# Optimization experiments

Hardware: AMD Instinct MI355X
Metric: run time of the kernel (lower is better)

## Reference

```python
import jax, jax.numpy as jnp
import numpy as np

TAU = 2.0   # membrane time constant
V_TH = 0.5  # firing threshold

@jax.custom_vjp
def spike_fn(v):
    return jnp.where(v > 0, 1.0, 0.0)

def _spike_fwd(v):
    return spike_fn(v), v

def _spike_bwd(v, g):
    # atan surrogate gradient (alpha=2): d s / d v = 1 / (1 + (pi*v)^2)
    sg = 1.0 / (1.0 + (jnp.pi * v) ** 2)
    return (g * sg,)

spike_fn.defvjp(_spike_fwd, _spike_bwd)


def setup_inputs() -> dict:
    key = jax.random.key(0)
    # [batch, neurons, time] -- time on axis 2, matching moveaxis(x, 2, 0)
    x = jax.random.normal(key, (32, 16384, 100), dtype=jnp.float32)
    return {"x": x}


def reference(x):
    x_seq = jnp.moveaxis(x, 2, 0)  # [T, B, N]
    decay = 1.0 - 1.0 / TAU

    def scan_fn(v, x_t):
        v = v * decay + x_t            # leaky integrate
        s = spike_fn(v - V_TH)         # fire
        v = v - s * V_TH               # soft reset
        return v, s

    v_init = jnp.zeros_like(x_seq[0])
    _, spikes = jax.lax.scan(scan_fn, v_init, x_seq)
    return jnp.moveaxis(spikes, 0, 2)  # [B, N, T]
```

## Files before the change

### kernel.cpp

```cpp
#include <hip/hip_runtime.h>


#define T_STEPS 100
#define T_VEC   25
#define ROWS    64
#define CA      12
#define CB      13
#define LSTRIDE 13
#define DECAY   0.5f
#define VTH     0.5f

typedef float vfloat4 __attribute__((ext_vector_type(4)));

__global__ __launch_bounds__(64, 3) void lif_kernel(const float* __restrict__ x,
                                                    float* __restrict__ out,
                                                    int n_rows) {
    __shared__ vfloat4 tile[ROWS * LSTRIDE];
    __shared__ unsigned int bits[ROWS * 4];

    const int lane = threadIdx.x;
    const int row0 = blockIdx.x * ROWS;
    const int gf0 = row0 * T_VEC;
    const int total_f4 = n_rows * T_VEC;

    const vfloat4* __restrict__ xb = reinterpret_cast<const vfloat4*>(x);
    const vfloat4 vzero = {0.0f, 0.0f, 0.0f, 0.0f};

    {
        vfloat4 st[CA];
        #pragma unroll
        for (int k = 0; k < CA; ++k) {
            int f = k * 64 + lane;
            int r = f / CA, c = f % CA;
            int g = gf0 + r * T_VEC + c;
            st[k] = (g < total_f4) ? xb[g] : vzero;
        }
        #pragma unroll
        for (int k = 0; k < CA; ++k) {
            int f = k * 64 + lane;
            int r = f / CA, c = f % CA;
            tile[r * LSTRIDE + c] = st[k];
        }
    }
    __syncthreads();

    vfloat4 sb[CB];
    #pragma unroll
    for (int k = 0; k < CB; ++k) {
        int f = k * 64 + lane;
        int r = f / CB, c = f % CB;
        int g = gf0 + r * T_VEC + CA + c;
        sb[k] = (g < total_f4) ? xb[g] : vzero;
    }
    __builtin_amdgcn_sched_barrier(0);

    unsigned int pk0 = 0, pk1 = 0, pk2 = 0, pk3 = 0;
    float v = 0.0f;
    #pragma unroll
    for (int c = 0; c < CA; ++c) {
        vfloat4 xs = tile[lane * LSTRIDE + c];
        #pragma unroll
        for (int k = 0; k < 4; ++k) {
            v = v * DECAY + xs[k];
            bool s = (v - VTH > 0.0f);
            v -= s ? VTH : 0.0f;
            unsigned int bit = s ? 1u : 0u;
            const int b = c * 4 + k;
            if (b < 32) pk0 |= bit << b;
            else        pk1 |= bit << (b - 32);
        }
    }
    __syncthreads();

    #pragma unroll
    for (int k = 0; k < CB; ++k) {
        int f = k * 64 + lane;
        int r = f / CB, c = f % CB;
        tile[r * LSTRIDE + c] = sb[k];
    }
    __syncthreads();

    #pragma unroll
    for (int c = 0; c < CB; ++c) {
        vfloat4 xs = tile[lane * LSTRIDE + c];
        #pragma unroll
        for (int k = 0; k < 4; ++k) {
            v = v * DECAY + xs[k];
            bool s = (v - VTH > 0.0f);
            v -= s ? VTH : 0.0f;
            unsigned int bit = s ? 1u : 0u;
            const int b = 48 + c * 4 + k;
            if (b < 64)      pk1 |= bit << (b - 32);
            else if (b < 96) pk2 |= bit << (b - 64);
            else             pk3 |= bit << (b - 96);
        }
    }

    {
        uint4 w; w.x = pk0; w.y = pk1; w.z = pk2; w.w = pk3;
        reinterpret_cast<uint4*>(bits)[lane] = w;
    }
    __syncthreads();

    vfloat4* __restrict__ ob = reinterpret_cast<vfloat4*>(out);
    #pragma unroll
    for (int i = 0; i < T_VEC; ++i) {
        int f = i * 64 + lane;
        int g = gf0 + f;
        if (g < total_f4) {
            int r  = f / T_VEC;
            int c4 = f % T_VEC;
            unsigned int word = bits[r * 4 + (c4 >> 3)];
            int shift = (c4 & 7) * 4;
            unsigned int nib = (word >> shift) & 0xFu;
            vfloat4 s;
            s.x = (nib & 1u) ? 1.0f : 0.0f;
            s.y = (nib & 2u) ? 1.0f : 0.0f;
            s.z = (nib & 4u) ? 1.0f : 0.0f;
            s.w = (nib & 8u) ? 1.0f : 0.0f;
            ob[g] = s;
        }
    }
}

extern "C" void kernel_launch(void* const* d_in, const int* in_sizes, int n_in,
                              void* d_out, int out_size, void* d_ws, size_t ws_size,
                              hipStream_t stream) {
    const float* x = (const float*)d_in[0];
    float* out = (float*)d_out;

    int n_rows = in_sizes[0] / T_STEPS;
    int grid = (n_rows + ROWS - 1) / ROWS;

    lif_kernel<<<grid, ROWS, 0, stream>>>(x, out, n_rows);
}
```

Baseline: 91.28 us.

## Split LIF into bit-packing walk kernel and separate spike expansion kernel

Splits the single fused kernel into two. The first runs the recurrence and writes packed spike bits per row to the workspace. The second, launched with 256-thread blocks, expands those bits into float output with grid-strided coalesced stores. The aim is to separate the latency-bound serial scan from the bandwidth-bound output write, so each can use its own launch shape. The cost is an extra launch and a round trip through the workspace; the fused path is kept as a fallback when the workspace is too small.

```diff
diff --git a/kernel.cpp b/kernel.cpp
--- a/kernel.cpp
+++ b/kernel.cpp
@@ -12,6 +12,117 @@
 
 typedef float vfloat4 __attribute__((ext_vector_type(4)));
 
+__global__ __launch_bounds__(64, 3) void lif_walk(const float* __restrict__ x,
+                                                  uint4* __restrict__ bitsg,
+                                                  int n_rows) {
+    __shared__ vfloat4 tile[ROWS * LSTRIDE];
+
+    const int lane = threadIdx.x;
+    const int row0 = blockIdx.x * ROWS;
+    const int gf0 = row0 * T_VEC;
+    const int total_f4 = n_rows * T_VEC;
+
+    const vfloat4* __restrict__ xb = reinterpret_cast<const vfloat4*>(x);
+    const vfloat4 vzero = {0.0f, 0.0f, 0.0f, 0.0f};
+
+    {
+        vfloat4 st[CA];
+        #pragma unroll
+        for (int k = 0; k < CA; ++k) {
+            int f = k * 64 + lane;
+            int r = f / CA, c = f % CA;
+            int g = gf0 + r * T_VEC + c;
+            st[k] = (g < total_f4) ? xb[g] : vzero;
+        }
+        #pragma unroll
+        for (int k = 0; k < CA; ++k) {
+            int f = k * 64 + lane;
+            int r = f / CA, c = f % CA;
+            tile[r * LSTRIDE + c] = st[k];
+        }
+    }
+    __syncthreads();
+
+    vfloat4 sb[CB];
+    #pragma unroll
+    for (int k = 0; k < CB; ++k) {
+        int f = k * 64 + lane;
+        int r = f / CB, c = f % CB;
+        int g = gf0 + r * T_VEC + CA + c;
+        sb[k] = (g < total_f4) ? xb[g] : vzero;
+    }
+    __builtin_amdgcn_sched_barrier(0);
+
+    unsigned int pk0 = 0, pk1 = 0, pk2 = 0, pk3 = 0;
+    float v = 0.0f;
+    #pragma unroll
+    for (int c = 0; c < CA; ++c) {
+        vfloat4 xs = tile[lane * LSTRIDE + c];
+        #pragma unroll
+        for (int k = 0; k < 4; ++k) {
+            v = v * DECAY + xs[k];
+            bool s = (v - VTH > 0.0f);
+            v -= s ? VTH : 0.0f;
+            unsigned int bit = s ? 1u : 0u;
+            const int b = c * 4 + k;
+            if (b < 32) pk0 |= bit << b;
+            else        pk1 |= bit << (b - 32);
+        }
+    }
+    __syncthreads();
+
+    #pragma unroll
+    for (int k = 0; k < CB; ++k) {
+        int f = k * 64 + lane;
+        int r = f / CB, c = f % CB;
+        tile[r * LSTRIDE + c] = sb[k];
+    }
+    __syncthreads();
+
+    #pragma unroll
+    for (int c = 0; c < CB; ++c) {
+        vfloat4 xs = tile[lane * LSTRIDE + c];
+        #pragma unroll
+        for (int k = 0; k < 4; ++k) {
+            v = v * DECAY + xs[k];
+            bool s = (v - VTH > 0.0f);
+            v -= s ? VTH : 0.0f;
+            unsigned int bit = s ? 1u : 0u;
+            const int b = 48 + c * 4 + k;
+            if (b < 64)      pk1 |= bit << (b - 32);
+            else if (b < 96) pk2 |= bit << (b - 64);
+            else             pk3 |= bit << (b - 96);
+        }
+    }
+
+    if (row0 + lane < n_rows) {
+        uint4 w; w.x = pk0; w.y = pk1; w.z = pk2; w.w = pk3;
+        bitsg[row0 + lane] = w;
+    }
+}
+
+__global__ __launch_bounds__(256) void lif_expand(const unsigned int* __restrict__ bw,
+                                                  vfloat4* __restrict__ ob,
+                                                  int total_f4, int nthreads) {
+    const int gtid = blockIdx.x * 256 + threadIdx.x;
+    #pragma unroll
+    for (int i = 0; i < T_VEC; ++i) {
+        int f = i * nthreads + gtid;
+        if (f < total_f4) {
+            int r  = f / T_VEC;
+            int c4 = f % T_VEC;
+            unsigned int word = bw[r * 4 + (c4 >> 3)];
+            unsigned int nib = (word >> ((c4 & 7) * 4)) & 0xFu;
+            vfloat4 s;
+            s.x = (nib & 1u) ? 1.0f : 0.0f;
+            s.y = (nib & 2u) ? 1.0f : 0.0f;
+            s.z = (nib & 4u) ? 1.0f : 0.0f;
+            s.w = (nib & 8u) ? 1.0f : 0.0f;
+            ob[f] = s;
+        }
+    }
+}
+
 __global__ __launch_bounds__(64, 3) void lif_kernel(const float* __restrict__ x,
                                                     float* __restrict__ out,
                                                     int n_rows) {
@@ -111,8 +222,7 @@
             int r  = f / T_VEC;
             int c4 = f % T_VEC;
             unsigned int word = bits[r * 4 + (c4 >> 3)];
-            int shift = (c4 & 7) * 4;
-            unsigned int nib = (word >> shift) & 0xFu;
+            unsigned int nib = (word >> ((c4 & 7) * 4)) & 0xFu;
             vfloat4 s;
             s.x = (nib & 1u) ? 1.0f : 0.0f;
             s.y = (nib & 2u) ? 1.0f : 0.0f;
@@ -130,7 +240,18 @@
     float* out = (float*)d_out;
 
     int n_rows = in_sizes[0] / T_STEPS;
-    int grid = (n_rows + ROWS - 1) / ROWS;
-
-    lif_kernel<<<grid, ROWS, 0, stream>>>(x, out, n_rows);
-}
+    int total_f4 = n_rows * T_VEC;
+    int grid1 = (n_rows + ROWS - 1) / ROWS;
+
+    size_t need = (size_t)n_rows * 16;
+    if (ws_size >= need) {
+        int nthreads_goal = (total_f4 + T_VEC - 1) / T_VEC;
+        int grid2 = (nthreads_goal + 255) / 256;
+        int nthreads = grid2 * 256;
+        lif_walk<<<grid1, ROWS, 0, stream>>>(x, (uint4*)d_ws, n_rows);
+        lif_expand<<<grid2, 256, 0, stream>>>((const unsigned int*)d_ws,
+                                              (vfloat4*)out, total_f4, nthreads);
+    } else {
+        lif_kernel<<<grid1, ROWS, 0, stream>>>(x, out, n_rows);
+    }
+}
```

Measured after the change: 99.58 us. +9.1%, slower.
